# Performance work log

Hardware: AMD Instinct MI355X
Metric: run time of the kernel (lower is better)

Reference implementation:

```python
import jax, jax.numpy as jnp
import numpy as np

# Dims (match init_kwargs)
T, C, RF, L = 32, 1, 64, 4096   # timesteps, inchannels, rf_size, length
K2 = 512                        # out_channels of self.ec
KWTA = 8
THRESH2 = 0.2                   # thresholds[1]
# inhibition_radius = 0 -> only per-feature inhibition in the winner loop


def setup_inputs() -> dict:
    key = jax.random.key(0)
    k1, k2 = jax.random.split(key)
    # spike-wave style input in [0,1)
    rec_field = jax.random.uniform(k1, (T, C, RF, L), dtype=jnp.float32)
    fan_in = C * RF * L
    weight = jax.random.normal(k2, (K2, C, RF, L), dtype=jnp.float32) / np.float32(np.sqrt(fan_in))
    return {"rec_field": rec_field, "weight": weight}


def reference(rec_field, weight):
    # LocalConvolution with kernel == full input -> single output location:
    # out[t, o, 0, 0] = sum_{c,h,w} rec_field[t,c,h,w] * weight[o,c,h,w]
    out = jnp.einsum('tchw,ochw->to', rec_field, weight)[:, :, None, None]  # (T, K2, 1, 1)

    # sf.fire(out, thresh2, True): zero potentials strictly below threshold
    pot = jnp.where(out < THRESH2, jnp.zeros_like(out), out)
    spikes = jnp.sign(pot)  # pot >= 0 after thresholding -> spikes in {0,1}

    # sf.get_k_winners(pot, kwta, inhibition_radius): spikes = pot.sign()
    n_t = spikes.shape[0]
    # index of earliest spike time (SpykeTorch cumulative-spike convention)
    first = jnp.clip((n_t - spikes.sum(axis=0, keepdims=True)).astype(jnp.int32), 0, n_t - 1)
    values = jnp.take_along_axis(pot, first, axis=0)          # (1, K2, 1, 1)
    trunc = spikes * values                                   # propagate earliest potential
    v = trunc.max() * n_t                                     # large offset so spiking neurons dominate
    trunc = trunc + spikes * v
    total = trunc.sum(axis=0)[:, 0, 0]                        # (K2,) -- spatial dims are 1x1

    # iterative k-WTA with per-feature inhibition (inhibition_radius=0; spatial is 1x1)
    sel = jnp.zeros((K2,), dtype=bool)
    t = total
    for _ in range(KWTA):  # small static loop
        idx = jnp.argmax(t)
        valid = t[idx] != 0          # original breaks when max == 0; totals are >= 0
        sel = sel.at[idx].set(sel[idx] | valid)
        t = t.at[idx].set(0.0)       # inhibit winning feature

    coef = sel.astype(pot.dtype)[None, :, None, None]
    return jnp.sign(pot * coef)  # (T, K2, 1, 1)
```

## Files before the change

### kernel.cpp

```cpp
#include <hip/hip_runtime.h>

#define TT    32
#define KDIM  262144
#define NFEAT 512
#define NF_BLOCK 16
#define FPT   4
#define BK    256

__global__ __launch_bounds__(256, 2)
void gemm_partial(const float* __restrict__ x, const float* __restrict__ w,
                  float* __restrict__ partial, int KC) {
    __shared__ float xs[TT][BK];

    const int tid  = threadIdx.x;
    const int wave = tid >> 6;
    const int lane = tid & 63;
    const int ftile  = blockIdx.x;
    const int kchunk = blockIdx.y;
    const int f0 = ftile * NF_BLOCK + wave * FPT;
    const size_t kbase = (size_t)kchunk * (size_t)KC;

    float acc[FPT][TT];
#pragma unroll
    for (int j = 0; j < FPT; ++j)
#pragma unroll
        for (int t = 0; t < TT; ++t) acc[j][t] = 0.f;

    const float* wp[FPT];
#pragma unroll
    for (int j = 0; j < FPT; ++j)
        wp[j] = w + (size_t)(f0 + j) * KDIM + kbase + (size_t)(lane << 2);

    float4 wv[FPT];
#pragma unroll
    for (int j = 0; j < FPT; ++j) wv[j] = *(const float4*)(wp[j]);

    for (int ks = 0; ks < KC; ks += BK) {
        float4 xr[8];
#pragma unroll
        for (int r = 0; r < 8; ++r) {
            const int t = r * 4 + wave;
            xr[r] = *(const float4*)(x + (size_t)t * KDIM + kbase + ks + (lane << 2));
        }
        __syncthreads();
#pragma unroll
        for (int r = 0; r < 8; ++r)
            *(float4*)(&xs[r * 4 + wave][lane << 2]) = xr[r];
        __syncthreads();

        const bool more = (ks + BK) < KC;
        float4 wn[FPT];
        if (more) {
#pragma unroll
            for (int j = 0; j < FPT; ++j)
                wn[j] = *(const float4*)(wp[j] + ks + BK);
        }

#pragma unroll
        for (int t = 0; t < TT; ++t) {
            const float4 xv = *(const float4*)(&xs[t][lane << 2]);
#pragma unroll
            for (int j = 0; j < FPT; ++j) {
                acc[j][t] += wv[j].x * xv.x;
                acc[j][t] += wv[j].y * xv.y;
                acc[j][t] += wv[j].z * xv.z;
                acc[j][t] += wv[j].w * xv.w;
            }
        }

        if (more) {
#pragma unroll
            for (int j = 0; j < FPT; ++j) wv[j] = wn[j];
        }
    }

#pragma unroll
    for (int j = 0; j < FPT; ++j) {
#pragma unroll
        for (int t = 0; t < TT; ++t) {
            float v = acc[j][t];
            v += __shfl_xor(v, 32, 64);
            v += __shfl_xor(v, 16, 64);
            v += __shfl_xor(v,  8, 64);
            v += __shfl_xor(v,  4, 64);
            v += __shfl_xor(v,  2, 64);
            v += __shfl_xor(v,  1, 64);
            acc[j][t] = v;
        }
    }

    if (lane == 0) {
#pragma unroll
        for (int j = 0; j < FPT; ++j) {
            float* p = partial + ((size_t)kchunk * NFEAT + (f0 + j)) * TT;
#pragma unroll
            for (int t = 0; t < TT; t += 4)
                *(float4*)(p + t) = make_float4(acc[j][t], acc[j][t+1],
                                                acc[j][t+2], acc[j][t+3]);
        }
    }
}

__global__ __launch_bounds__(256)
void reduce_chunks(const float* __restrict__ partial, int nkc,
                   float* __restrict__ potraw) {
    const int id = blockIdx.x * 256 + threadIdx.x;
    float s = 0.f;
    for (int c = 0; c < nkc; ++c)
        s += partial[(size_t)c * (NFEAT * TT) + id];
    potraw[id] = s;
}

__global__ __launch_bounds__(512)
void finalize(const float* __restrict__ potraw, float* __restrict__ out) {
    const int o = threadIdx.x;

    float pot[TT];
#pragma unroll
    for (int t = 0; t < TT; ++t) {
        const float s = potraw[o * TT + t];
        pot[t] = (s < 0.2f) ? 0.f : s;
    }

    int cnt = 0;
#pragma unroll
    for (int t = 0; t < TT; ++t) cnt += (pot[t] > 0.f) ? 1 : 0;

    int first = TT - cnt;
    if (first > TT - 1) first = TT - 1;
    float value = 0.f;
#pragma unroll
    for (int t = 0; t < TT; ++t)
        if (t == first) value = pot[t];

    __shared__ float rv[NFEAT];
    __shared__ int   ri[NFEAT];
    __shared__ float tot[NFEAT];
    __shared__ int   sel[NFEAT];

    rv[o] = (cnt > 0) ? value : 0.f;
    __syncthreads();
    for (int s = 256; s > 0; s >>= 1) {
        if (o < s) rv[o] = fmaxf(rv[o], rv[o + s]);
        __syncthreads();
    }
    const float v = rv[0] * (float)TT;
    __syncthreads();

    tot[o] = (float)cnt * (value + v);
    sel[o] = 0;
    __syncthreads();

    for (int it = 0; it < 8; ++it) {
        rv[o] = tot[o]; ri[o] = o;
        __syncthreads();
        for (int s = 256; s > 0; s >>= 1) {
            if (o < s) {
                const float v2 = rv[o + s];
                const int   i2 = ri[o + s];
                if (v2 > rv[o] || (v2 == rv[o] && i2 < ri[o])) {
                    rv[o] = v2; ri[o] = i2;
                }
            }
            __syncthreads();
        }
        if (o == 0) {
            if (rv[0] != 0.f) sel[ri[0]] = 1;
            tot[ri[0]] = 0.f;
        }
        __syncthreads();
    }

#pragma unroll
    for (int t = 0; t < TT; ++t)
        out[t * NFEAT + o] = (sel[o] && pot[t] > 0.f) ? 1.f : 0.f;
}

extern "C" void kernel_launch(void* const* d_in, const int* in_sizes, int n_in,
                              void* d_out, int out_size, void* d_ws, size_t ws_size,
                              hipStream_t stream) {
    const float* x = (const float*)d_in[0];
    const float* w = (const float*)d_in[1];
    float* out = (float*)d_out;

    int nkc = 32;
    while (nkc > 1 &&
           ((size_t)nkc * NFEAT * TT * sizeof(float) + NFEAT * TT * sizeof(float)) > ws_size)
        nkc >>= 1;
    const int KC = KDIM / nkc;

    float* partial = (float*)d_ws;
    float* potraw  = partial + (size_t)nkc * NFEAT * TT;

    gemm_partial<<<dim3(32, nkc), 256, 0, stream>>>(x, w, partial, KC);
    reduce_chunks<<<(NFEAT * TT) / 256, 256, 0, stream>>>(partial, nkc, potraw);
    finalize<<<1, NFEAT, 0, stream>>>(potraw, out);
}
```

Before: 1.001 ms.

## Retile GEMM across feature/time wave groups with async double-buffered LDS loads

```diff
diff --git a/kernel.cpp b/kernel.cpp
--- a/kernel.cpp
+++ b/kernel.cpp
@@ -3,81 +3,83 @@
 #define TT    32
 #define KDIM  262144
 #define NFEAT 512
-#define NF_BLOCK 16
-#define FPT   4
+#define NFB   16
+#define FPT   8
+#define TPT   8
 #define BK    256
 
-__global__ __launch_bounds__(256, 2)
+__device__ __forceinline__ void async_ld16(const float* g, float* lds_row) {
+    __builtin_amdgcn_global_load_lds(
+        (const __attribute__((address_space(1))) unsigned int*)g,
+        (__attribute__((address_space(3))) unsigned int*)lds_row, 16, 0, 0);
+}
+
+__global__ __launch_bounds__(512, 2)
 void gemm_partial(const float* __restrict__ x, const float* __restrict__ w,
                   float* __restrict__ partial, int KC) {
-    __shared__ float xs[TT][BK];
+    __shared__ float xs[2][TT][BK];
 
     const int tid  = threadIdx.x;
+    const int lane = tid & 63;
     const int wave = tid >> 6;
-    const int lane = tid & 63;
+    const int fgrp = wave & 1;
+    const int tgrp = wave >> 1;
     const int ftile  = blockIdx.x;
     const int kchunk = blockIdx.y;
-    const int f0 = ftile * NF_BLOCK + wave * FPT;
+    const int f0 = ftile * NFB + fgrp * FPT;
+    const int t0 = tgrp * TPT;
     const size_t kbase = (size_t)kchunk * (size_t)KC;
 
-    float acc[FPT][TT];
+    float acc[FPT][TPT];
 #pragma unroll
     for (int j = 0; j < FPT; ++j)
 #pragma unroll
-        for (int t = 0; t < TT; ++t) acc[j][t] = 0.f;
+        for (int t = 0; t < TPT; ++t) acc[j][t] = 0.f;
 
-    const float* wp[FPT];
+    const float* wbase = w + (size_t)f0 * KDIM + kbase + (lane << 2);
+    const float* xbase = x + kbase + (lane << 2);
+
 #pragma unroll
-    for (int j = 0; j < FPT; ++j)
-        wp[j] = w + (size_t)(f0 + j) * KDIM + kbase + (size_t)(lane << 2);
+    for (int r = 0; r < 4; ++r) {
+        const int t = wave * 4 + r;
+        async_ld16(xbase + (size_t)t * KDIM, &xs[0][t][0]);
+    }
 
-    float4 wv[FPT];
-#pragma unroll
-    for (int j = 0; j < FPT; ++j) wv[j] = *(const float4*)(wp[j]);
-
+    int cur = 0;
     for (int ks = 0; ks < KC; ks += BK) {
-        float4 xr[8];
-#pragma unroll
-        for (int r = 0; r < 8; ++r) {
-            const int t = r * 4 + wave;
-            xr[r] = *(const float4*)(x + (size_t)t * KDIM + kbase + ks + (lane << 2));
-        }
-        __syncthreads();
-#pragma unroll
-        for (int r = 0; r < 8; ++r)
-            *(float4*)(&xs[r * 4 + wave][lane << 2]) = xr[r];
         __syncthreads();
 
-        const bool more = (ks + BK) < KC;
-        float4 wn[FPT];
-        if (more) {
+        if (ks + BK < KC) {
 #pragma unroll
-            for (int j = 0; j < FPT; ++j)
-                wn[j] = *(const float4*)(wp[j] + ks + BK);
-        }
-
-#pragma unroll
-        for (int t = 0; t < TT; ++t) {
-            const float4 xv = *(const float4*)(&xs[t][lane << 2]);
-#pragma unroll
-            for (int j = 0; j < FPT; ++j) {
-                acc[j][t] += wv[j].x * xv.x;
-                acc[j][t] += wv[j].y * xv.y;
-                acc[j][t] += wv[j].z * xv.z;
-                acc[j][t] += wv[j].w * xv.w;
+            for (int r = 0; r < 4; ++r) {
+                const int t = wave * 4 + r;
+                async_ld16(xbase + (size_t)t * KDIM + (ks + BK), &xs[cur ^ 1][t][0]);
             }
         }
 
-        if (more) {
+        float4 wv[FPT];
 #pragma unroll
-            for (int j = 0; j < FPT; ++j) wv[j] = wn[j];
+        for (int j = 0; j < FPT; ++j)
+            wv[j] = *(const float4*)(wbase + (size_t)j * KDIM + ks);
+
+#pragma unroll
+        for (int t = 0; t < TPT; ++t) {
+            const float4 xv = *(const float4*)(&xs[cur][t0 + t][lane << 2]);
+#pragma unroll
+            for (int j = 0; j < FPT; ++j) {
+                acc[j][t] = fmaf(wv[j].x, xv.x, acc[j][t]);
+                acc[j][t] = fmaf(wv[j].y, xv.y, acc[j][t]);
+                acc[j][t] = fmaf(wv[j].z, xv.z, acc[j][t]);
+                acc[j][t] = fmaf(wv[j].w, xv.w, acc[j][t]);
+            }
         }
+        cur ^= 1;
     }
 
 #pragma unroll
     for (int j = 0; j < FPT; ++j) {
 #pragma unroll
-        for (int t = 0; t < TT; ++t) {
+        for (int t = 0; t < TPT; ++t) {
             float v = acc[j][t];
             v += __shfl_xor(v, 32, 64);
             v += __shfl_xor(v, 16, 64);
@@ -92,11 +94,9 @@
     if (lane == 0) {
 #pragma unroll
         for (int j = 0; j < FPT; ++j) {
-            float* p = partial + ((size_t)kchunk * NFEAT + (f0 + j)) * TT;
-#pragma unroll
-            for (int t = 0; t < TT; t += 4)
-                *(float4*)(p + t) = make_float4(acc[j][t], acc[j][t+1],
-                                                acc[j][t+2], acc[j][t+3]);
+            float* p = partial + ((size_t)kchunk * NFEAT + (f0 + j)) * TT + t0;
+            *(float4*)(p)     = make_float4(acc[j][0], acc[j][1], acc[j][2], acc[j][3]);
+            *(float4*)(p + 4) = make_float4(acc[j][4], acc[j][5], acc[j][6], acc[j][7]);
         }
     }
 }
@@ -185,14 +185,14 @@
 
     int nkc = 32;
     while (nkc > 1 &&
-           ((size_t)nkc * NFEAT * TT * sizeof(float) + NFEAT * TT * sizeof(float)) > ws_size)
+           ((size_t)(nkc + 1) * NFEAT * TT * sizeof(float)) > ws_size)
         nkc >>= 1;
     const int KC = KDIM / nkc;
 
     float* partial = (float*)d_ws;
     float* potraw  = partial + (size_t)nkc * NFEAT * TT;
 
-    gemm_partial<<<dim3(32, nkc), 256, 0, stream>>>(x, w, partial, KC);
+    gemm_partial<<<dim3(32, nkc), 512, 0, stream>>>(x, w, partial, KC);
     reduce_chunks<<<(NFEAT * TT) / 256, 256, 0, stream>>>(partial, nkc, potraw);
     finalize<<<1, NFEAT, 0, stream>>>(potraw, out);
 }
```

New measurement: 889.1 us. 11.2% less time.
